# Kernel optimization log

Hardware: AMD Instinct MI355X
Metric: run time of the kernel (lower is better)

Reference implementation:

```python
import math
import jax, jax.numpy as jnp
import numpy as np

B, S, D = 2, 4096, 2048
H, DK, DV, SEG = 16, 128, 128, 512
DH = 8192
LN_EPS = 1e-5


def setup_inputs() -> dict:
    key = jax.random.key(0)
    ks = jax.random.split(key, 12)
    s = 0.02
    return {
        "x": jax.random.normal(ks[0], (B, S, D), dtype=jnp.float32),
        "Wq": jax.random.normal(ks[1], (D, H * DK), dtype=jnp.float32) * s,
        "Wk": jax.random.normal(ks[2], (D, H * DK), dtype=jnp.float32) * s,
        "Wv": jax.random.normal(ks[3], (D, H * DV), dtype=jnp.float32) * s,
        "Wo": jax.random.normal(ks[4], (H * DV, D), dtype=jnp.float32) * s,
        "betas": jax.random.normal(ks[5], (1, H, 1, DV), dtype=jnp.float32),
        "W1": jax.random.normal(ks[6], (D, DH), dtype=jnp.float32) * s,
        "b1": jnp.zeros((DH,), dtype=jnp.float32),
        "W2": jax.random.normal(ks[7], (DH, D), dtype=jnp.float32) * s,
        "b2": jnp.zeros((D,), dtype=jnp.float32),
        "ln_g": jnp.ones((D,), dtype=jnp.float32),
        "ln_b": jnp.zeros((D,), dtype=jnp.float32),
    }


def _split_segments(t, n_seg, hd):
    # (B, S, H*hd) -> (n_seg, B, H, SEG, hd)
    t = t.reshape(B, n_seg, SEG, H, hd)
    return jnp.transpose(t, (1, 0, 3, 2, 4))


def reference(x, Wq, Wk, Wv, Wo, betas, W1, b1, W2, b2, ln_g, ln_b):
    n_seg = S // SEG
    q = _split_segments(x @ Wq, n_seg, DK)
    k = _split_segments(x @ Wk, n_seg, DK)
    v = _split_segments(x @ Wv, n_seg, DV)

    causal_mask = jnp.tril(jnp.ones((SEG, SEG), dtype=bool))
    gate = jax.nn.sigmoid(betas)  # (1,H,1,DV)
    scale = 1.0 / math.sqrt(DK)

    def step(carry, qkv):
        mem, z = carry  # mem: (B,H,DK,DV), z: (B,H,DK,1)
        qs, ks_, vs = qkv  # (B,H,SEG,dk/dv)
        sig_q = jax.nn.elu(qs) + 1.0
        # standard SDP attention within the segment
        scores = jnp.einsum('bhsd,bhtd->bhst', qs, ks_) * scale
        scores = jnp.where(causal_mask, scores, -jnp.inf)
        att_dot = jnp.einsum('bhst,bhtv->bhsv', jax.nn.softmax(scores, axis=-1), vs)
        # memory retrieval (normalized linear attention)
        att_mem = jnp.einsum('bhsd,bhdv->bhsv', sig_q, mem) / jnp.einsum('bhsd,bhdo->bhso', sig_q, z)
        # linear memory update
        sig_k = jax.nn.elu(ks_) + 1.0
        mem = mem + jnp.einsum('bhsd,bhsv->bhdv', sig_k, vs)
        z = z + jnp.sum(sig_k, axis=2)[..., None]
        att = gate * att_mem + (1.0 - gate) * att_dot  # (B,H,SEG,DV)
        return (mem, z), att

    mem0 = jnp.zeros((B, H, DK, DV), dtype=x.dtype)
    z0 = jnp.ones((B, H, DK, 1), dtype=x.dtype) / DK
    _, outs = jax.lax.scan(step, (mem0, z0), (q, k, v))  # (n_seg,B,H,SEG,DV)

    att = jnp.transpose(outs, (1, 0, 3, 2, 4)).reshape(B, S, H * DV)
    attn_out = att @ Wo
    # MLP (dropout = 0)
    h = jax.nn.relu(attn_out @ W1 + b1)
    y = h @ W2 + b2
    # residual + LayerNorm
    res = y + x
    mu = jnp.mean(res, axis=-1, keepdims=True)
    var = jnp.var(res, axis=-1, keepdims=True)
    return (res - mu) / jnp.sqrt(var + LN_EPS) * ln_g + ln_b
```

## Files before the change

### kernel.cpp

```cpp
#include <hip/hip_runtime.h>

typedef short s16x8 __attribute__((ext_vector_type(8)));
typedef unsigned short u16x8 __attribute__((ext_vector_type(8)));
typedef unsigned short u16x4 __attribute__((ext_vector_type(4)));
typedef float f32x4 __attribute__((ext_vector_type(4)));

#define CB 2
#define CS 4096
#define CD 2048
#define CH 16
#define CSEG 512
#define CDH 8192

__device__ __forceinline__ unsigned short f2b(float f) {
  union { float f; unsigned u; } v; v.f = f;
  unsigned r = v.u + 0x7fffu + ((v.u >> 16) & 1u);
  return (unsigned short)(r >> 16);
}
__device__ __forceinline__ float b2f(unsigned short b) {
  union { unsigned u; float f; } v; v.u = ((unsigned)b) << 16;
  return v.f;
}
__device__ __forceinline__ f32x4 mfma16(s16x8 a, s16x8 b, f32x4 c) {
  return __builtin_amdgcn_mfma_f32_16x16x32_bf16(a, b, c, 0, 0, 0);
}
__device__ __forceinline__ void async16(const unsigned short* g, unsigned short* l) {
  __builtin_amdgcn_global_load_lds((const __attribute__((address_space(1))) void*)g,
                                   (__attribute__((address_space(3))) void*)l, 16, 0, 0);
}

__global__ void convert_bf16_k(const float* __restrict__ in, unsigned short* __restrict__ out) {
  size_t i = ((size_t)blockIdx.x * 256 + threadIdx.x) * 4;
  f32x4 v = *(const f32x4*)(in + i);
  u16x4 o;
  #pragma unroll
  for (int e = 0; e < 4; e++) o[e] = f2b(v[e]);
  *(u16x4*)(out + i) = o;
}

__global__ void transpose_bf16_k(const float* __restrict__ in, unsigned short* __restrict__ out,
                                 int R, int C) {
  __shared__ float tile[32][33];
  int c0 = blockIdx.x * 32, r0 = blockIdx.y * 32;
  int tx = threadIdx.x & 31, ty = threadIdx.x >> 5;
  #pragma unroll
  for (int i = 0; i < 32; i += 8)
    tile[ty + i][tx] = in[(size_t)(r0 + ty + i) * C + c0 + tx];
  __syncthreads();
  #pragma unroll
  for (int i = 0; i < 32; i += 8)
    out[(size_t)(c0 + ty + i) * R + r0 + tx] = f2b(tile[tx][ty + i]);
}

__global__ void transpose_kv_k(const unsigned short* __restrict__ kb,
                               const unsigned short* __restrict__ vb,
                               unsigned short* __restrict__ KT,
                               unsigned short* __restrict__ VT) {
  __shared__ unsigned short kt_[64][72];
  __shared__ unsigned short vt_[64][72];
  const int t = threadIdx.x;
  const int r0 = blockIdx.x * 64, c0 = blockIdx.y * 64;
  {
    int row = t >> 2, cc = (t & 3) * 16;
    size_t g = (size_t)(r0 + row) * CD + c0 + cc;
    #pragma unroll
    for (int u = 0; u < 2; u++) {
      u16x8 kv = *(const u16x8*)(kb + g + u * 8);
      u16x8 vv = *(const u16x8*)(vb + g + u * 8);
      u16x8 ko;
      #pragma unroll
      for (int e = 0; e < 8; e++) {
        float f = b2f(kv[e]);
        ko[e] = f2b(f > 0.f ? f + 1.f : __expf(f));
      }
      *(u16x8*)&kt_[row][cc + u * 8] = ko;
      *(u16x8*)&vt_[row][cc + u * 8] = vv;
    }
  }
  __syncthreads();
  {
    int vc = t >> 2, s0 = (t & 3) * 16;
    int c = c0 + vc;
    int h = c >> 7, v = c & 127;
    int b = r0 >> 12, sbase = (r0 & 4095) + s0;
    size_t obase = ((size_t)((b * 16 + h) * 128 + v) << 12) + sbase;
    u16x8 wk0, wk1, wv0, wv1;
    #pragma unroll
    for (int e = 0; e < 8; e++) {
      wk0[e] = kt_[s0 + e][vc];      wv0[e] = vt_[s0 + e][vc];
      wk1[e] = kt_[s0 + 8 + e][vc];  wv1[e] = vt_[s0 + 8 + e][vc];
    }
    *(u16x8*)&KT[obase] = wk0;  *(u16x8*)&KT[obase + 8] = wk1;
    *(u16x8*)&VT[obase] = wv0;  *(u16x8*)&VT[obase + 8] = wv1;
  }
}

template <int EPI>
__global__ void gemm_bt(const unsigned short* __restrict__ A,
                        const unsigned short* __restrict__ BT,
                        const float* __restrict__ bias,
                        void* __restrict__ Cp, int M, int N, int K) {
  __shared__ unsigned short As[128 * 32];
  __shared__ unsigned short Bs[128 * 32];
  const int t = threadIdx.x, wave = t >> 6, lane = t & 63;
  const int fr = lane & 15, fq = (lane >> 4) * 8;
  const int nbx = gridDim.x, nby = gridDim.y;
  int flat = blockIdx.x + blockIdx.y * nbx;
  int stripe = flat / (8 * nby);
  int rem = flat % (8 * nby);
  const int m0 = (stripe * 8 + (rem & 7)) * 128, n0 = (rem >> 3) * 128;
  const int wr = (wave >> 1) * 64, wc = (wave & 1) * 64;
  const int srow = lane >> 2, scol = (lane & 3) * 8;

  f32x4 acc[4][4] = {};

  const unsigned short* Ag = A + (size_t)(m0 + wave * 32 + srow) * K + scol;
  const unsigned short* Bg = BT + (size_t)(n0 + wave * 32 + srow) * K + scol;
  unsigned short* Al = As + (wave * 32) * 32;
  unsigned short* Bl = Bs + (wave * 32) * 32;
  const size_t r16 = (size_t)16 * K;

  for (int kk = 0; kk < K; kk += 32) {
    __syncthreads();
    async16(Ag + kk, Al);
    async16(Ag + kk + r16, Al + 16 * 32);
    async16(Bg + kk, Bl);
    async16(Bg + kk + r16, Bl + 16 * 32);
    __syncthreads();
    s16x8 af[4], bfr[4];
    #pragma unroll
    for (int i = 0; i < 4; i++) af[i] = *(const s16x8*)&As[(wr + i * 16 + fr) * 32 + fq];
    #pragma unroll
    for (int j = 0; j < 4; j++) bfr[j] = *(const s16x8*)&Bs[(wc + j * 16 + fr) * 32 + fq];
    #pragma unroll
    for (int i = 0; i < 4; i++)
      #pragma unroll
      for (int j = 0; j < 4; j++)
        acc[i][j] = mfma16(af[i], bfr[j], acc[i][j]);
  }

  const int er = (lane >> 4) * 4, ec = lane & 15;
  #pragma unroll
  for (int i = 0; i < 4; i++) {
    int row = m0 + wr + i * 16 + er;
    #pragma unroll
    for (int j = 0; j < 4; j++) {
      int col = n0 + wc + j * 16 + ec;
      float bv = (EPI >= 2) ? bias[col] : 0.f;
      #pragma unroll
      for (int r = 0; r < 4; r++) {
        float v = acc[i][j][r];
        size_t idx = (size_t)(row + r) * N + col;
        if (EPI == 1) ((unsigned short*)Cp)[idx] = f2b(v);
        else if (EPI == 2) { v += bv; ((unsigned short*)Cp)[idx] = f2b(v > 0.f ? v : 0.f); }
        else { v += bv; ((unsigned short*)Cp)[idx] = f2b(v); }
      }
    }
  }
}

__global__ void kvsum_k(const unsigned short* __restrict__ KT, const unsigned short* __restrict__ VT,
                        float* __restrict__ memsegT, float* __restrict__ zseg) {
  __shared__ unsigned short As[128 * 32];
  __shared__ unsigned short Bs[128 * 32];
  const int seg = blockIdx.x, b = blockIdx.y, h = blockIdx.z;
  const int bh = b * 16 + h;
  const int t = threadIdx.x, wave = t >> 6, lane = t & 63;
  const int fr = lane & 15, fq = (lane >> 4) * 8;
  const int wr = (wave >> 1) * 64, wc = (wave & 1) * 64;

  f32x4 acc[4][4] = {};
  const size_t sbase = (size_t)seg * 512;
  const unsigned short* Ag = VT + ((size_t)(bh * 128 + wave * 32 + (lane >> 2)) << 12) + sbase + (lane & 3) * 8;
  const unsigned short* Bg = KT + ((size_t)(bh * 128 + wave * 32 + (lane >> 2)) << 12) + sbase + (lane & 3) * 8;
  unsigned short* Al = As + (wave * 32) * 32;
  unsigned short* Bl = Bs + (wave * 32) * 32;
  const size_t r16 = (size_t)16 << 12;

  for (int kk = 0; kk < 512; kk += 32) {
    __syncthreads();
    async16(Ag + kk, Al);
    async16(Ag + kk + r16, Al + 16 * 32);
    async16(Bg + kk, Bl);
    async16(Bg + kk + r16, Bl + 16 * 32);
    __syncthreads();
    s16x8 af[4], bfr[4];
    #pragma unroll
    for (int i = 0; i < 4; i++) af[i] = *(const s16x8*)&As[(wr + i * 16 + fr) * 32 + fq];
    #pragma unroll
    for (int j = 0; j < 4; j++) bfr[j] = *(const s16x8*)&Bs[(wc + j * 16 + fr) * 32 + fq];
    #pragma unroll
    for (int i = 0; i < 4; i++)
      #pragma unroll
      for (int j = 0; j < 4; j++)
        acc[i][j] = mfma16(af[i], bfr[j], acc[i][j]);
  }

  const size_t obase = (size_t)((seg * 2 + b) * 16 + h) * 16384;
  const int er = (lane >> 4) * 4, ec = lane & 15;
  #pragma unroll
  for (int i = 0; i < 4; i++)
    #pragma unroll
    for (int j = 0; j < 4; j++)
      #pragma unroll
      for (int r = 0; r < 4; r++)
        memsegT[obase + (size_t)(wr + i * 16 + er + r) * 128 + wc + j * 16 + ec] = acc[i][j][r];

  if (t < 128) {
    const unsigned short* zp = KT + ((size_t)(bh * 128 + t) << 12) + sbase;
    float z = 0.f;
    #pragma unroll 4
    for (int u = 0; u < 64; u++) {
      u16x8 kv = *(const u16x8*)(zp + u * 8);
      #pragma unroll
      for (int e = 0; e < 8; e++) z += b2f(kv[e]);
    }
    zseg[(size_t)((seg * 2 + b) * 16 + h) * 128 + t] = z;
  }
}

__global__ void prefix_k(const float* __restrict__ memsegT, const float* __restrict__ zseg,
                         unsigned short* __restrict__ memPT, float* __restrict__ zP) {
  const int bh = blockIdx.x, t = threadIdx.x;
  for (int e = t; e < 16384; e += 256) {
    float a = 0.f;
    #pragma unroll
    for (int s = 0; s < 8; s++) {
      size_t idx = (size_t)(s * 32 + bh) * 16384 + e;
      memPT[idx] = f2b(a);
      a += memsegT[idx];
    }
  }
  if (t < 128) {
    float a = 1.f / 128.f;
    #pragma unroll
    for (int s = 0; s < 8; s++) {
      size_t idx = (size_t)(s * 32 + bh) * 128 + t;
      zP[idx] = a;
      a += zseg[idx];
    }
  }
}

#define PD 136
#define PPS 40
__global__ void attn_k(const unsigned short* __restrict__ qb,
                       const unsigned short* __restrict__ kb,
                       const unsigned short* __restrict__ VT,
                       const unsigned short* __restrict__ memPT,
                       const float* __restrict__ zPv,
                       const float* __restrict__ betas,
                       unsigned short* __restrict__ att) {
  const int qt = blockIdx.x, seg = blockIdx.y, bh = blockIdx.z;
  const int b = bh >> 4, h = bh & 15;
  const int t = threadIdx.x, wave = t >> 6, lane = t & 63;
  const int fr = lane & 15, quad = lane >> 4, fq = quad * 8;

  __shared__ unsigned short Qs[64 * PD];
  __shared__ unsigned short SB[64 * PD];
  __shared__ unsigned short KB[32 * PD];
  __shared__ unsigned short VTs[128 * PPS];
  __shared__ float denomS[64];
  __shared__ float dpart[4][64];
  __shared__ float zPs[128];

  unsigned short* SQ = SB;
  unsigned short* Ps = SB;

  const size_t qrow0 = (size_t)b * CS + (size_t)seg * CSEG + (size_t)qt * 64;
  const size_t mbase = (size_t)(seg * 32 + bh) * 16384;
  const size_t vtbase = ((size_t)(bh * 128) << 12) + (size_t)seg * 512;

  {
    int row = t >> 2, c0 = (t & 3) * 32;
    const unsigned short* src = qb + (qrow0 + row) * (size_t)CD + (size_t)h * 128 + c0;
    #pragma unroll
    for (int u = 0; u < 4; u++) {
      u16x8 qv = *(const u16x8*)(src + u * 8);
      u16x8 qo, so;
      #pragma unroll
      for (int e = 0; e < 8; e++) {
        float f = b2f(qv[e]);
        qo[e] = f2b(f * 0.08838834764831845f);
        so[e] = f2b(f > 0.f ? f + 1.f : __expf(f));
      }
      *(u16x8*)&Qs[row * PD + c0 + u * 8] = qo;
      *(u16x8*)&SQ[row * PD + c0 + u * 8] = so;
    }
    if (t < 128) zPs[t] = zPv[(size_t)(seg * 32 + bh) * 128 + t];
  }
  __syncthreads();

  {
    int row = t & 63, part = t >> 6;
    float s = 0.f;
    #pragma unroll
    for (int i = 0; i < 32; i++) {
      int d = part * 32 + i;
      s += b2f(SQ[row * PD + d]) * zPs[d];
    }
    dpart[part][row] = s;
  }
  __syncthreads();
  if (t < 64) denomS[t] = dpart[0][t] + dpart[1][t] + dpart[2][t] + dpart[3][t];

  f32x4 om[8] = {};
  for (int qd = 0; qd < 4; qd++) {
    __syncthreads();
    {
      int row = t >> 3, c0 = (t & 7) * 16;
      const unsigned short* msrc = memPT + mbase + (size_t)(qd * 32 + row) * 128 + c0;
      *(u16x8*)&KB[row * PD + c0] = *(const u16x8*)msrc;
      *(u16x8*)&KB[row * PD + c0 + 8] = *(const u16x8*)(msrc + 8);
    }
    __syncthreads();
    #pragma unroll
    for (int jj = 0; jj < 2; jj++)
      #pragma unroll
      for (int kf = 0; kf < 4; kf++) {
        s16x8 a = *(const s16x8*)&SQ[(wave * 16 + fr) * PD + kf * 32 + fq];
        s16x8 bb = *(const s16x8*)&KB[(jj * 16 + fr) * PD + kf * 32 + fq];
        om[qd * 2 + jj] = mfma16(a, bb, om[qd * 2 + jj]);
      }
  }

  f32x4 od[8] = {};
  float mrow[4], lrow[4];
  #pragma unroll
  for (int r = 0; r < 4; r++) { mrow[r] = -1e30f; lrow[r] = 0.f; }

  const int nkt = qt * 2 + 2;
  for (int kt = 0; kt < nkt; kt++) {
    __syncthreads();
    {
      int row = t >> 3, c0 = (t & 7) * 16;
      size_t g = ((size_t)b * CS + (size_t)seg * CSEG + (size_t)kt * 32 + row) * CD + (size_t)h * 128 + c0;
      *(u16x8*)&KB[row * PD + c0] = *(const u16x8*)(kb + g);
      *(u16x8*)&KB[row * PD + c0 + 8] = *(const u16x8*)(kb + g + 8);
      int v = t >> 1, sc = (t & 1) * 16;
      const unsigned short* vsrc = VT + vtbase + ((size_t)v << 12) + kt * 32 + sc;
      *(u16x8*)&VTs[v * PPS + sc] = *(const u16x8*)vsrc;
      *(u16x8*)&VTs[v * PPS + sc + 8] = *(const u16x8*)(vsrc + 8);
    }
    __syncthreads();

    f32x4 sc[2] = {};
    #pragma unroll
    for (int kf = 0; kf < 4; kf++) {
      s16x8 a = *(const s16x8*)&Qs[(wave * 16 + fr) * PD + kf * 32 + fq];
      #pragma unroll
      for (int nt = 0; nt < 2; nt++) {
        s16x8 bb = *(const s16x8*)&KB[(nt * 16 + fr) * PD + kf * 32 + fq];
        sc[nt] = mfma16(a, bb, sc[nt]);
      }
    }

    if (kt >= 2 * qt) {
      #pragma unroll
      for (int nt = 0; nt < 2; nt++)
        #pragma unroll
        for (int r = 0; r < 4; r++) {
          int qi = qt * 64 + wave * 16 + quad * 4 + r;
          int ki = kt * 32 + nt * 16 + fr;
          if (ki > qi) sc[nt][r] = -1e30f;
        }
    }

    float al[4], pv[2][4];
    #pragma unroll
    for (int r = 0; r < 4; r++) {
      float mx = fmaxf(sc[0][r], sc[1][r]);
      #pragma unroll
      for (int xm = 8; xm >= 1; xm >>= 1) mx = fmaxf(mx, __shfl_xor(mx, xm, 64));
      float mn = fmaxf(mrow[r], mx);
      al[r] = __expf(mrow[r] - mn);
      mrow[r] = mn;
      float ps = 0.f;
      #pragma unroll
      for (int nt = 0; nt < 2; nt++) {
        float p = __expf(sc[nt][r] - mn);
        pv[nt][r] = p;
        ps += p;
      }
      #pragma unroll
      for (int xm = 8; xm >= 1; xm >>= 1) ps += __shfl_xor(ps, xm, 64);
      lrow[r] = lrow[r] * al[r] + ps;
    }
    #pragma unroll
    for (int j = 0; j < 8; j++)
      #pragma unroll
      for (int r = 0; r < 4; r++) od[j][r] *= al[r];

    #pragma unroll
    for (int nt = 0; nt < 2; nt++)
      #pragma unroll
      for (int r = 0; r < 4; r++)
        Ps[(wave * 16 + quad * 4 + r) * PPS + nt * 16 + fr] = f2b(pv[nt][r]);

    s16x8 a = *(const s16x8*)&Ps[(wave * 16 + fr) * PPS + fq];
    #pragma unroll
    for (int j = 0; j < 8; j++) {
      s16x8 bb = *(const s16x8*)&VTs[(j * 16 + fr) * PPS + fq];
      od[j] = mfma16(a, bb, od[j]);
    }
  }

  #pragma unroll
  for (int j = 0; j < 8; j++) {
    int vcol = j * 16 + fr;
    float g = 1.f / (1.f + __expf(-betas[h * 128 + vcol]));
    #pragma unroll
    for (int r = 0; r < 4; r++) {
      int rowl = wave * 16 + quad * 4 + r;
      float amem = om[j][r] / denomS[rowl];
      float adot = od[j][r] / lrow[r];
      att[(qrow0 + rowl) * (size_t)CD + (size_t)h * 128 + vcol] = f2b(g * amem + (1.f - g) * adot);
    }
  }
}

__global__ void ln_k(const unsigned short* __restrict__ y, const float* __restrict__ x,
                     const float* __restrict__ gam, const float* __restrict__ bet,
                     float* __restrict__ out) {
  const int row = blockIdx.x, t = threadIdx.x;
  const int lane = t & 63, wave = t >> 6;
  const unsigned short* yr = y + (size_t)row * CD;
  const float* xr = x + (size_t)row * CD;
  float v[8];
  float s = 0.f, ss = 0.f;
  u16x8 a8 = *(const u16x8*)(yr + t * 8);
  #pragma unroll
  for (int u = 0; u < 2; u++) {
    f32x4 c = *(const f32x4*)(xr + t * 8 + u * 4);
    #pragma unroll
    for (int e = 0; e < 4; e++) {
      float r = b2f(a8[u * 4 + e]) + c[e];
      v[u * 4 + e] = r; s += r; ss += r * r;
    }
  }
  #pragma unroll
  for (int off = 32; off >= 1; off >>= 1) {
    s += __shfl_xor(s, off, 64);
    ss += __shfl_xor(ss, off, 64);
  }
  __shared__ float red[8];
  if (lane == 0) { red[wave] = s; red[4 + wave] = ss; }
  __syncthreads();
  s = red[0] + red[1] + red[2] + red[3];
  ss = red[4] + red[5] + red[6] + red[7];
  const float mu = s * (1.f / 2048.f);
  const float var = ss * (1.f / 2048.f) - mu * mu;
  const float rs = rsqrtf(var + 1e-5f);
  #pragma unroll
  for (int u = 0; u < 2; u++)
    #pragma unroll
    for (int e = 0; e < 4; e++) {
      int c = t * 8 + u * 4 + e;
      out[(size_t)row * CD + c] = (v[u * 4 + e] - mu) * rs * gam[c] + bet[c];
    }
}

extern "C" void kernel_launch(void* const* d_in, const int* in_sizes, int n_in,
                              void* d_out, int out_size, void* d_ws, size_t ws_size,
                              hipStream_t stream) {
  const float* xf   = (const float*)d_in[0];
  const float* Wq   = (const float*)d_in[1];
  const float* Wk   = (const float*)d_in[2];
  const float* Wv   = (const float*)d_in[3];
  const float* Wo   = (const float*)d_in[4];
  const float* bet  = (const float*)d_in[5];
  const float* W1   = (const float*)d_in[6];
  const float* b1   = (const float*)d_in[7];
  const float* W2   = (const float*)d_in[8];
  const float* b2   = (const float*)d_in[9];
  const float* lng  = (const float*)d_in[10];
  const float* lnb  = (const float*)d_in[11];
  float* out = (float*)d_out;

  const size_t MB = 1024ull * 1024ull;
  char* w = (char*)d_ws;
  unsigned short* qbuf  = (unsigned short*)(w + 0 * MB);
  unsigned short* kbuf  = (unsigned short*)(w + 32 * MB);
  unsigned short* vbuf  = (unsigned short*)(w + 64 * MB);
  unsigned short* xb    = (unsigned short*)(w + 96 * MB);
  unsigned short* VTg   = (unsigned short*)(w + 96 * MB);
  unsigned short* KTg   = (unsigned short*)(w + 128 * MB);
  unsigned short* attb  = (unsigned short*)(w + 128 * MB);
  float*          msegT = (float*)(w + 64 * MB);
  unsigned short* memPT = (unsigned short*)(w + 80 * MB);
  float*          zsegb = (float*)(w + 88 * MB);
  float*          zPb   = (float*)(w + 89 * MB);
  unsigned short* aob   = (unsigned short*)(w + 0 * MB);
  unsigned short* hb    = (unsigned short*)(w + 32 * MB);
  unsigned short* ybb   = (unsigned short*)(w + 0 * MB);
  unsigned short* W1T   = (unsigned short*)(w + 160 * MB);
  unsigned short* W2T   = (unsigned short*)(w + 160 * MB);
  unsigned short* WqT   = (unsigned short*)(w + 192 * MB);
  unsigned short* WkT   = (unsigned short*)(w + 200 * MB);
  unsigned short* WvT   = (unsigned short*)(w + 208 * MB);
  unsigned short* WoT   = (unsigned short*)(w + 216 * MB);

  convert_bf16_k<<<dim3(16384), 256, 0, stream>>>(xf, xb);
  transpose_bf16_k<<<dim3(64, 64), 256, 0, stream>>>(Wq, WqT, 2048, 2048);
  transpose_bf16_k<<<dim3(64, 64), 256, 0, stream>>>(Wk, WkT, 2048, 2048);
  transpose_bf16_k<<<dim3(64, 64), 256, 0, stream>>>(Wv, WvT, 2048, 2048);
  transpose_bf16_k<<<dim3(64, 64), 256, 0, stream>>>(Wo, WoT, 2048, 2048);
  transpose_bf16_k<<<dim3(256, 64), 256, 0, stream>>>(W1, W1T, 2048, 8192);

  gemm_bt<1><<<dim3(64, 16), 256, 0, stream>>>(xb, WqT, nullptr, qbuf, 8192, 2048, 2048);
  gemm_bt<1><<<dim3(64, 16), 256, 0, stream>>>(xb, WkT, nullptr, kbuf, 8192, 2048, 2048);
  gemm_bt<1><<<dim3(64, 16), 256, 0, stream>>>(xb, WvT, nullptr, vbuf, 8192, 2048, 2048);

  transpose_kv_k<<<dim3(128, 32), 256, 0, stream>>>(kbuf, vbuf, KTg, VTg);
  kvsum_k<<<dim3(8, 2, 16), 256, 0, stream>>>(KTg, VTg, msegT, zsegb);
  prefix_k<<<dim3(32), 256, 0, stream>>>(msegT, zsegb, memPT, zPb);
  attn_k<<<dim3(8, 8, 32), 256, 0, stream>>>(qbuf, kbuf, VTg, memPT, zPb, bet, attb);

  gemm_bt<1><<<dim3(64, 16), 256, 0, stream>>>(attb, WoT, nullptr, aob, 8192, 2048, 2048);
  gemm_bt<2><<<dim3(64, 64), 256, 0, stream>>>(aob, W1T, b1, hb, 8192, 8192, 2048);
  transpose_bf16_k<<<dim3(64, 256), 256, 0, stream>>>(W2, W2T, 8192, 2048);
  gemm_bt<4><<<dim3(64, 16), 256, 0, stream>>>(hb, W2T, b2, ybb, 8192, 2048, 8192);
  ln_k<<<dim3(8192), 256, 0, stream>>>(ybb, xf, lng, lnb, out);
}
```

Baseline: 1.482 ms.

## Replace 128x128 GEMM with 256x256 double-buffered, swizzled, ping-pong scheduled GEMM

Replaces the simple 128x128-tile GEMM, which issues a single async load and two barriers per K-step of 32, with a 256x256 tile, 512-thread kernel. The new kernel uses a K-step of 64, double-buffered LDS with loads prefetched two tiles ahead, an XOR-swizzled LDS layout to avoid bank conflicts, and four quadrant MFMA phases separated by barriers and setprio. The goal is to raise arithmetic intensity and overlap global loads with MFMA work in every projection and MLP GEMM. In exchange it uses 128KB of LDS per block and more registers, which lowers occupancy, and the hand-placed waitcnt scheduling is fragile.

New measurement: 1.281 ms. 13.6% less time.

```diff
diff --git a/kernel.cpp b/kernel.cpp
--- a/kernel.cpp
+++ b/kernel.cpp
@@ -96,67 +96,150 @@
 }
 
 template <int EPI>
-__global__ void gemm_bt(const unsigned short* __restrict__ A,
-                        const unsigned short* __restrict__ BT,
-                        const float* __restrict__ bias,
-                        void* __restrict__ Cp, int M, int N, int K) {
-  __shared__ unsigned short As[128 * 32];
-  __shared__ unsigned short Bs[128 * 32];
+__global__ __launch_bounds__(512, 2) void gemm256(const unsigned short* __restrict__ A,
+                                                  const unsigned short* __restrict__ BT,
+                                                  const float* __restrict__ bias,
+                                                  unsigned short* __restrict__ C,
+                                                  int M, int N, int K) {
+  __shared__ unsigned short As[2 * 16384];
+  __shared__ unsigned short Bs[2 * 16384];
+
   const int t = threadIdx.x, wave = t >> 6, lane = t & 63;
-  const int fr = lane & 15, fq = (lane >> 4) * 8;
-  const int nbx = gridDim.x, nby = gridDim.y;
-  int flat = blockIdx.x + blockIdx.y * nbx;
-  int stripe = flat / (8 * nby);
-  int rem = flat % (8 * nby);
-  const int m0 = (stripe * 8 + (rem & 7)) * 128, n0 = (rem >> 3) * 128;
-  const int wr = (wave >> 1) * 64, wc = (wave & 1) * 64;
-  const int srow = lane >> 2, scol = (lane & 3) * 8;
-
-  f32x4 acc[4][4] = {};
-
-  const unsigned short* Ag = A + (size_t)(m0 + wave * 32 + srow) * K + scol;
-  const unsigned short* Bg = BT + (size_t)(n0 + wave * 32 + srow) * K + scol;
-  unsigned short* Al = As + (wave * 32) * 32;
-  unsigned short* Bl = Bs + (wave * 32) * 32;
-  const size_t r16 = (size_t)16 * K;
-
-  for (int kk = 0; kk < K; kk += 32) {
-    __syncthreads();
-    async16(Ag + kk, Al);
-    async16(Ag + kk + r16, Al + 16 * 32);
-    async16(Bg + kk, Bl);
-    async16(Bg + kk + r16, Bl + 16 * 32);
-    __syncthreads();
-    s16x8 af[4], bfr[4];
-    #pragma unroll
-    for (int i = 0; i < 4; i++) af[i] = *(const s16x8*)&As[(wr + i * 16 + fr) * 32 + fq];
-    #pragma unroll
-    for (int j = 0; j < 4; j++) bfr[j] = *(const s16x8*)&Bs[(wc + j * 16 + fr) * 32 + fq];
-    #pragma unroll
-    for (int i = 0; i < 4; i++)
-      #pragma unroll
-      for (int j = 0; j < 4; j++)
-        acc[i][j] = mfma16(af[i], bfr[j], acc[i][j]);
-  }
-
-  const int er = (lane >> 4) * 4, ec = lane & 15;
-  #pragma unroll
-  for (int i = 0; i < 4; i++) {
-    int row = m0 + wr + i * 16 + er;
-    #pragma unroll
-    for (int j = 0; j < 4; j++) {
-      int col = n0 + wc + j * 16 + ec;
-      float bv = (EPI >= 2) ? bias[col] : 0.f;
-      #pragma unroll
-      for (int r = 0; r < 4; r++) {
-        float v = acc[i][j][r];
-        size_t idx = (size_t)(row + r) * N + col;
-        if (EPI == 1) ((unsigned short*)Cp)[idx] = f2b(v);
-        else if (EPI == 2) { v += bv; ((unsigned short*)Cp)[idx] = f2b(v > 0.f ? v : 0.f); }
-        else { v += bv; ((unsigned short*)Cp)[idx] = f2b(v); }
-      }
-    }
-  }
+  const int fr = lane & 15, quad = lane >> 4;
+  const int wm = wave >> 2, wn = wave & 3;
+  const int wave8 = wave * 8;
+
+  const int nwg = (int)gridDim.x;
+  const int q8 = nwg >> 3;
+  const int wg = (blockIdx.x & 7) * q8 + (blockIdx.x >> 3);
+  const int nN = N >> 8;
+  const int stripe = wg / (8 * nN), rem = wg % (8 * nN);
+  const int m0 = (stripe * 8 + (rem & 7)) << 8;
+  const int n0 = (rem >> 3) << 8;
+
+  const int NT = K >> 6;
+
+  const int scol = ((t & 7) ^ ((t >> 3) & 7)) * 8;
+  const unsigned short* Asrc = A + (size_t)(m0 + (t >> 3)) * K + scol;
+  const unsigned short* Bsrc = BT + (size_t)(n0 + (t >> 3)) * K + scol;
+
+  const int sw0 = ((quad ^ (fr & 7)) * 8);
+  const int sw1 = (((4 + quad) ^ (fr & 7)) * 8);
+  const int arow = wm * 128 + fr;
+  const int brow = wn * 64 + fr;
+
+  f32x4 c00[4][2] = {}, c01[4][2] = {}, c11[4][2] = {}, c10[4][2] = {};
+  s16x8 aC[4][2], b0f[2][2], b1f[2][2];
+
+#define STG2(SRC, LB, HR, KT)                                                            \
+  do {                                                                                   \
+    async16((SRC) + (size_t)(HR) * K + (size_t)(KT) * 64, (LB) + ((HR) + wave8) * 64);   \
+    async16((SRC) + (size_t)((HR) + 64) * K + (size_t)(KT) * 64,                         \
+            (LB) + ((HR) + 64 + wave8) * 64);                                            \
+  } while (0)
+
+#define LDA4(DST, BASE, ROFF)                                          \
+  _Pragma("unroll") for (int m_ = 0; m_ < 4; m_++) {                   \
+    const unsigned short* p_ = (BASE) + (size_t)(arow + (ROFF) + m_ * 16) * 64; \
+    DST[m_][0] = *(const s16x8*)(p_ + sw0);                            \
+    DST[m_][1] = *(const s16x8*)(p_ + sw1);                            \
+  }
+
+#define LDB2(DST, BASE, ROFF)                                          \
+  _Pragma("unroll") for (int n_ = 0; n_ < 2; n_++) {                   \
+    const unsigned short* p_ = (BASE) + (size_t)(brow + (ROFF) + n_ * 16) * 64; \
+    DST[n_][0] = *(const s16x8*)(p_ + sw0);                            \
+    DST[n_][1] = *(const s16x8*)(p_ + sw1);                            \
+  }
+
+#define MFMA_Q(CC, AV, BV)                                             \
+  _Pragma("unroll") for (int k_ = 0; k_ < 2; k_++)                     \
+  _Pragma("unroll") for (int m_ = 0; m_ < 4; m_++)                     \
+  _Pragma("unroll") for (int n_ = 0; n_ < 2; n_++)                     \
+      CC[m_][n_] = mfma16(AV[m_][k_], BV[n_][k_], CC[m_][n_]);
+
+  {
+    unsigned short* A0 = As;           unsigned short* B0 = Bs;
+    unsigned short* A1 = As + 16384;   unsigned short* B1 = Bs + 16384;
+    STG2(Bsrc, B0, 0, 0);   STG2(Bsrc, B0, 128, 0);
+    STG2(Asrc, A0, 0, 0);   STG2(Asrc, A0, 128, 0);
+    STG2(Bsrc, B1, 0, 1);   STG2(Bsrc, B1, 128, 1);
+    STG2(Asrc, A1, 0, 1);   STG2(Asrc, A1, 128, 1);
+  }
+  asm volatile("s_waitcnt vmcnt(8)" ::: "memory");
+  __builtin_amdgcn_s_barrier();
+
+  for (int tt = 0; tt < NT; tt++) {
+    const int cur = tt & 1;
+    unsigned short* Ac = As + (cur << 14);
+    unsigned short* Bc = Bs + (cur << 14);
+    const int k2 = (tt + 2 < NT) ? tt + 2 : NT - 1;
+
+    LDA4(aC, Ac, 0)
+    LDB2(b0f, Bc, 0)
+    __builtin_amdgcn_s_barrier();
+    asm volatile("s_waitcnt lgkmcnt(0)" ::: "memory");
+    __builtin_amdgcn_sched_barrier(0);
+    __builtin_amdgcn_s_setprio(1);
+    MFMA_Q(c00, aC, b0f)
+    __builtin_amdgcn_s_setprio(0);
+    __builtin_amdgcn_s_barrier();
+
+    LDB2(b1f, Bc, 32)
+    __builtin_amdgcn_s_barrier();
+    asm volatile("s_waitcnt lgkmcnt(0)" ::: "memory");
+    __builtin_amdgcn_sched_barrier(0);
+    __builtin_amdgcn_s_setprio(1);
+    MFMA_Q(c01, aC, b1f)
+    __builtin_amdgcn_s_setprio(0);
+    __builtin_amdgcn_s_barrier();
+
+    LDA4(aC, Ac, 64)
+    STG2(Bsrc, Bc, 0, k2);
+    STG2(Bsrc, Bc, 128, k2);
+    __builtin_amdgcn_s_barrier();
+    asm volatile("s_waitcnt lgkmcnt(0)" ::: "memory");
+    __builtin_amdgcn_sched_barrier(0);
+    __builtin_amdgcn_s_setprio(1);
+    MFMA_Q(c11, aC, b1f)
+    __builtin_amdgcn_s_setprio(0);
+    __builtin_amdgcn_s_barrier();
+
+    asm volatile("s_waitcnt vmcnt(4)" ::: "memory");
+    STG2(Asrc, Ac, 0, k2);
+    STG2(Asrc, Ac, 128, k2);
+    __builtin_amdgcn_s_barrier();
+    __builtin_amdgcn_s_setprio(1);
+    MFMA_Q(c10, aC, b0f)
+    __builtin_amdgcn_s_setprio(0);
+    __builtin_amdgcn_s_barrier();
+  }
+
+  const int er = quad * 4;
+#define EPIQ(CC, MH, NH)                                               \
+  _Pragma("unroll") for (int m_ = 0; m_ < 4; m_++) {                   \
+    int row_ = m0 + wm * 128 + (MH)*64 + m_ * 16 + er;                 \
+    _Pragma("unroll") for (int n_ = 0; n_ < 2; n_++) {                 \
+      int col_ = n0 + wn * 64 + (NH)*32 + n_ * 16 + fr;                \
+      float bv_ = (EPI >= 2) ? bias[col_] : 0.f;                       \
+      _Pragma("unroll") for (int r_ = 0; r_ < 4; r_++) {               \
+        float v_ = CC[m_][n_][r_];                                     \
+        size_t idx_ = (size_t)(row_ + r_) * N + col_;                  \
+        if (EPI == 1) C[idx_] = f2b(v_);                               \
+        else if (EPI == 2) { v_ += bv_; C[idx_] = f2b(v_ > 0.f ? v_ : 0.f); } \
+        else { v_ += bv_; C[idx_] = f2b(v_); }                         \
+      }                                                                \
+    }                                                                  \
+  }
+  EPIQ(c00, 0, 0)
+  EPIQ(c01, 0, 1)
+  EPIQ(c11, 1, 1)
+  EPIQ(c10, 1, 0)
+#undef EPIQ
+#undef MFMA_Q
+#undef LDB2
+#undef LDA4
+#undef STG2
 }
 
 __global__ void kvsum_k(const unsigned short* __restrict__ KT, const unsigned short* __restrict__ VT,
@@ -507,18 +590,18 @@
   transpose_bf16_k<<<dim3(64, 64), 256, 0, stream>>>(Wo, WoT, 2048, 2048);
   transpose_bf16_k<<<dim3(256, 64), 256, 0, stream>>>(W1, W1T, 2048, 8192);
 
-  gemm_bt<1><<<dim3(64, 16), 256, 0, stream>>>(xb, WqT, nullptr, qbuf, 8192, 2048, 2048);
-  gemm_bt<1><<<dim3(64, 16), 256, 0, stream>>>(xb, WkT, nullptr, kbuf, 8192, 2048, 2048);
-  gemm_bt<1><<<dim3(64, 16), 256, 0, stream>>>(xb, WvT, nullptr, vbuf, 8192, 2048, 2048);
+  gemm256<1><<<dim3(256), 512, 0, stream>>>(xb, WqT, nullptr, qbuf, 8192, 2048, 2048);
+  gemm256<1><<<dim3(256), 512, 0, stream>>>(xb, WkT, nullptr, kbuf, 8192, 2048, 2048);
+  gemm256<1><<<dim3(256), 512, 0, stream>>>(xb, WvT, nullptr, vbuf, 8192, 2048, 2048);
 
   transpose_kv_k<<<dim3(128, 32), 256, 0, stream>>>(kbuf, vbuf, KTg, VTg);
   kvsum_k<<<dim3(8, 2, 16), 256, 0, stream>>>(KTg, VTg, msegT, zsegb);
   prefix_k<<<dim3(32), 256, 0, stream>>>(msegT, zsegb, memPT, zPb);
   attn_k<<<dim3(8, 8, 32), 256, 0, stream>>>(qbuf, kbuf, VTg, memPT, zPb, bet, attb);
 
-  gemm_bt<1><<<dim3(64, 16), 256, 0, stream>>>(attb, WoT, nullptr, aob, 8192, 2048, 2048);
-  gemm_bt<2><<<dim3(64, 64), 256, 0, stream>>>(aob, W1T, b1, hb, 8192, 8192, 2048);
+  gemm256<1><<<dim3(256), 512, 0, stream>>>(attb, WoT, nullptr, aob, 8192, 2048, 2048);
+  gemm256<2><<<dim3(1024), 512, 0, stream>>>(aob, W1T, b1, hb, 8192, 8192, 2048);
   transpose_bf16_k<<<dim3(64, 256), 256, 0, stream>>>(W2, W2T, 8192, 2048);
-  gemm_bt<4><<<dim3(64, 16), 256, 0, stream>>>(hb, W2T, b2, ybb, 8192, 2048, 8192);
+  gemm256<4><<<dim3(256), 512, 0, stream>>>(hb, W2T, b2, ybb, 8192, 2048, 8192);
   ln_k<<<dim3(8192), 256, 0, stream>>>(ybb, xf, lng, lnb, out);
 }
```
